# Kernel tuning notes

Measured on AMD Instinct MI355X. Metric: run time of the kernel, lower is better.

## Reference

```python
import jax, jax.numpy as jnp
import numpy as np

E = 2048      # embed_dim = qk_dim = v_dim = proj_dim
H = 16        # n_head
D = 128       # head_dim
ROT = 64      # rotary_dim (partial rotary: ROT < D)
PAD = 50257   # pad_token_id in select_at_last_token
EPS = 1e-5    # layer_norm_epsilon


def _sincos(T):
    # fixed_pos_embedding (GPT-J style): [T, ROT//2] each
    inv_freq = 1.0 / (10000.0 ** (jnp.arange(0, ROT, 2, dtype=jnp.float32) / ROT))
    ang = jnp.arange(T, dtype=jnp.float32)[:, None] * inv_freq[None, :]
    return jnp.sin(ang), jnp.cos(ang)


def _rope(x, sin, cos):
    # x: [B,T,H,ROT]; sin/cos: [T, ROT//2]; repeat_interleave(2) on last dim
    sin2 = jnp.repeat(sin, 2, axis=-1)[None, :, None, :]
    cos2 = jnp.repeat(cos, 2, axis=-1)[None, :, None, :]
    x1 = x[..., ::2]
    x2 = x[..., 1::2]
    rot = jnp.stack((-x2, x1), axis=-1).reshape(x.shape)  # rotate_every_two
    return x * cos2 + rot * sin2


def setup_inputs() -> dict:
    key = jax.random.key(0)
    ks = jax.random.split(key, 8)
    B, S = 8, 2048
    s = 0.02
    return {
        "hidden_states": jax.random.normal(ks[0], (B, S, E), jnp.float32),
        "input_ids_with_pads": jax.random.randint(ks[1], (B, S), 0, PAD),
        "ln_w": jnp.ones((E,), jnp.float32),
        "ln_b": jnp.zeros((E,), jnp.float32),
        "q_w": jax.random.normal(ks[2], (E, E), jnp.float32) * s,
        "q_b": jnp.zeros((E,), jnp.float32),
        "k_w": jax.random.normal(ks[3], (E, E), jnp.float32) * s,
        "k_b": jnp.zeros((E,), jnp.float32),
        "v_w": jax.random.normal(ks[4], (E, E), jnp.float32) * s,
        "v_b": jnp.zeros((E,), jnp.float32),
        "out_w": jax.random.normal(ks[5], (E, E), jnp.float32) * s,
        "out_b": jnp.zeros((E,), jnp.float32),
    }


def reference(hidden_states, input_ids_with_pads, ln_w, ln_b,
              q_w, q_b, k_w, k_b, v_w, v_b, out_w, out_b):
    B, S, _ = hidden_states.shape
    # LayerNorm
    mu = jnp.mean(hidden_states, axis=-1, keepdims=True)
    var = jnp.mean(jnp.square(hidden_states - mu), axis=-1, keepdims=True)
    hs = (hidden_states - mu) * jax.lax.rsqrt(var + EPS) * ln_w + ln_b
    # select_at_last_token: index of last non-pad token per row
    ix = jnp.argmax(jnp.cumsum((input_ids_with_pads != PAD).astype(jnp.int32), axis=1), axis=1)  # [B]
    h_last = jnp.take_along_axis(hs, ix[:, None, None], axis=1)  # [B,1,E]
    # projections (pool_to_vector: single query token)
    q = h_last @ q_w.T + q_b           # [B,1,E]
    k = hs @ k_w.T + k_b               # [B,S,E]
    v = hs @ v_w.T + v_b               # [B,S,E]
    # split heads; rotary layout keeps [B,T,H,D] for q,k
    q = q.reshape(B, 1, H, D)
    k = k.reshape(B, S, H, D)
    v = v.reshape(B, S, H, D).transpose(0, 2, 1, 3)  # [B,H,S,D]
    # partial rotary on first ROT dims (query at position 0, keys 0..S-1)
    sin, cos = _sincos(S)
    q = jnp.concatenate([_rope(q[..., :ROT], sin[:1], cos[:1]), q[..., ROT:]], axis=-1)
    k = jnp.concatenate([_rope(k[..., :ROT], sin, cos), k[..., ROT:]], axis=-1)
    q = q.transpose(0, 2, 1, 3)  # [B,H,1,D]
    k = k.transpose(0, 2, 1, 3)  # [B,H,S,D]
    # GPT-Neo _attn: no 1/sqrt(d) scaling; `bias` buffer is all-ones so the
    # causal mask is all-True and masked_bias is never applied.
    scores = jnp.einsum('bhqd,bhkd->bhqk', q, k)   # [B,H,1,S]
    attn = jax.nn.softmax(scores, axis=-1)
    out = jnp.einsum('bhqk,bhkd->bhqd', attn, v)   # [B,H,1,D]
    out = out.transpose(0, 2, 1, 3).reshape(B, 1, H * D)  # merge heads
    out = out @ out_w.T + out_b                    # out_proj
    return out[:, 0, :]                            # squeeze(-2): [B,E]
```

## Files before the change

kernel.cpp:

```cpp
#include <hip/hip_runtime.h>
#include <hip/hip_bf16.h>
#include <cstdint>
#include <cstddef>


using bf16x8 = __attribute__((ext_vector_type(8))) __bf16;
using f32x4  = __attribute__((ext_vector_type(4))) float;

__device__ __forceinline__ unsigned short f2bf(float f) {
  unsigned u = __float_as_uint(f);
  u += 0x7fffu + ((u >> 16) & 1u);
  return (unsigned short)(u >> 16);
}

__device__ __forceinline__ void gld16(const void* g, void* l) {
  __builtin_amdgcn_global_load_lds((__attribute__((address_space(1))) void*)g,
                                   (__attribute__((address_space(3))) void*)l,
                                   16, 0, 0);
}

#define FENCE() asm volatile("" ::: "memory")
#define SBAR()  { FENCE(); __builtin_amdgcn_s_barrier(); FENCE(); }
#define VM9()   asm volatile("s_waitcnt vmcnt(9)" ::: "memory")
#define VM8()   asm volatile("s_waitcnt vmcnt(8)" ::: "memory")
#define VM0()   asm volatile("s_waitcnt vmcnt(0)" ::: "memory")

__global__ __launch_bounds__(256) void prep_kernel(
    const float* __restrict__ hidden, const int* __restrict__ ids,
    const float* __restrict__ gw, const float* __restrict__ gb,
    const float* __restrict__ kw, unsigned short* __restrict__ hs,
    unsigned short* __restrict__ Wk, float2* __restrict__ tab,
    float* __restrict__ hl, float* __restrict__ Z) {
  const int blk = blockIdx.x, tid = threadIdx.x;
  const int wave = tid >> 6, lane = tid & 63;

  if (blk < 16384) {
    const size_t row = blk;
    const float* xr = hidden + row * 2048;
    float4 a = ((const float4*)xr)[tid];
    float4 b = ((const float4*)xr)[tid + 256];
    float s  = a.x + a.y + a.z + a.w + b.x + b.y + b.z + b.w;
    float ss = a.x*a.x + a.y*a.y + a.z*a.z + a.w*a.w +
               b.x*b.x + b.y*b.y + b.z*b.z + b.w*b.w;
    for (int m = 1; m < 64; m <<= 1) { s += __shfl_xor(s, m); ss += __shfl_xor(ss, m); }
    __shared__ float rs[4], rss[4];
    if (lane == 0) { rs[wave] = s; rss[wave] = ss; }
    __syncthreads();
    s  = rs[0] + rs[1] + rs[2] + rs[3];
    ss = rss[0] + rss[1] + rss[2] + rss[3];
    const float mu = s * (1.f / 2048.f);
    const float var = ss * (1.f / 2048.f) - mu * mu;
    const float r = rsqrtf(var + 1e-5f);
    const int i0 = tid * 4, i1 = 1024 + tid * 4;
    ushort4 p0 = {f2bf((a.x - mu) * r * gw[i0 + 0] + gb[i0 + 0]),
                  f2bf((a.y - mu) * r * gw[i0 + 1] + gb[i0 + 1]),
                  f2bf((a.z - mu) * r * gw[i0 + 2] + gb[i0 + 2]),
                  f2bf((a.w - mu) * r * gw[i0 + 3] + gb[i0 + 3])};
    ushort4 p1 = {f2bf((b.x - mu) * r * gw[i1 + 0] + gb[i1 + 0]),
                  f2bf((b.y - mu) * r * gw[i1 + 1] + gb[i1 + 1]),
                  f2bf((b.z - mu) * r * gw[i1 + 2] + gb[i1 + 2]),
                  f2bf((b.w - mu) * r * gw[i1 + 3] + gb[i1 + 3])};
    *(ushort4*)(hs + row * 2048 + i0) = p0;
    *(ushort4*)(hs + row * 2048 + i1) = p1;
  } else if (blk < 18432) {
    const size_t i4 = (size_t)(blk - 16384) * 256 + tid;
    const int r = (int)(i4 >> 9);
    const int col4 = (int)(i4 & 511);
    const size_t src4 = ((size_t)((r >> 6) * 128 + (r & 63))) * 512 + col4;
    float4 v = ((const float4*)kw)[src4];
    ushort4 o = {f2bf(v.x), f2bf(v.y), f2bf(v.z), f2bf(v.w)};
    ((ushort4*)Wk)[i4] = o;
  } else if (blk < 18688) {
    const int t = (blk - 18432) * 8 + (tid >> 5);
    const int i = tid & 31;
    const float inv = exp2f(-(float)i * (13.287712379549449f / 32.f));
    const float ang = (float)t * inv;
    tab[t * 32 + i] = make_float2(sinf(ang), cosf(ang));
  } else {
    const int b = blk - 18688;
    if (tid < 16) Z[b * 16 + tid] = 0.f;
    int best = -1;
    for (int t = tid; t < 2048; t += 256)
      if (ids[b * 2048 + t] != 50257) best = (t > best) ? t : best;
    for (int m = 1; m < 64; m <<= 1) {
      int o = __shfl_xor(best, m);
      best = (o > best) ? o : best;
    }
    __shared__ int rb[4];
    if (lane == 0) rb[wave] = best;
    __syncthreads();
    int ix = rb[0];
    for (int w = 1; w < 4; ++w) ix = (rb[w] > ix) ? rb[w] : ix;
    ix = (ix < 0) ? 0 : ix;
    const float* xr = hidden + ((size_t)b * 2048 + ix) * 2048;
    float4 a = ((const float4*)xr)[tid];
    float4 c = ((const float4*)xr)[tid + 256];
    float s  = a.x + a.y + a.z + a.w + c.x + c.y + c.z + c.w;
    float ss = a.x*a.x + a.y*a.y + a.z*a.z + a.w*a.w +
               c.x*c.x + c.y*c.y + c.z*c.z + c.w*c.w;
    for (int m = 1; m < 64; m <<= 1) { s += __shfl_xor(s, m); ss += __shfl_xor(ss, m); }
    __shared__ float rs2[4], rss2[4];
    if (lane == 0) { rs2[wave] = s; rss2[wave] = ss; }
    __syncthreads();
    s  = rs2[0] + rs2[1] + rs2[2] + rs2[3];
    ss = rss2[0] + rss2[1] + rss2[2] + rss2[3];
    const float mu = s * (1.f / 2048.f);
    const float var = ss * (1.f / 2048.f) - mu * mu;
    const float r = rsqrtf(var + 1e-5f);
    const int i0 = tid * 4, i1 = 1024 + tid * 4;
    float* yo = hl + (size_t)b * 2048;
    yo[i0 + 0] = (a.x - mu) * r * gw[i0 + 0] + gb[i0 + 0];
    yo[i0 + 1] = (a.y - mu) * r * gw[i0 + 1] + gb[i0 + 1];
    yo[i0 + 2] = (a.z - mu) * r * gw[i0 + 2] + gb[i0 + 2];
    yo[i0 + 3] = (a.w - mu) * r * gw[i0 + 3] + gb[i0 + 3];
    yo[i1 + 0] = (c.x - mu) * r * gw[i1 + 0] + gb[i1 + 0];
    yo[i1 + 1] = (c.y - mu) * r * gw[i1 + 1] + gb[i1 + 1];
    yo[i1 + 2] = (c.z - mu) * r * gw[i1 + 2] + gb[i1 + 2];
    yo[i1 + 3] = (c.w - mu) * r * gw[i1 + 3] + gb[i1 + 3];
  }
}

__global__ __launch_bounds__(256) void gemv8_kernel(const float* __restrict__ X,
                                                    const float* __restrict__ W,
                                                    const float* __restrict__ bias,
                                                    float* __restrict__ Y) {
  const int tid = threadIdx.x, lane = tid & 63, wave = tid >> 6;
  const int e = blockIdx.x * 4 + wave;
  const float* wr = W + (size_t)e * 2048;
  float p[8] = {0, 0, 0, 0, 0, 0, 0, 0};
#pragma unroll
  for (int it = 0; it < 8; ++it) {
    const int k = it * 256 + lane * 4;
    float4 wv = *(const float4*)(wr + k);
#pragma unroll
    for (int b = 0; b < 8; ++b) {
      float4 xv = *(const float4*)(X + b * 2048 + k);
      p[b] += wv.x * xv.x + wv.y * xv.y + wv.z * xv.z + wv.w * xv.w;
    }
  }
#pragma unroll
  for (int b = 0; b < 8; ++b)
    for (int m = 1; m < 64; m <<= 1) p[b] += __shfl_xor(p[b], m);
  if (lane == 0) {
    const float bb = bias[e];
#pragma unroll
    for (int b = 0; b < 8; ++b) Y[(size_t)b * 2048 + e] = p[b] + bb;
  }
}

__global__ __launch_bounds__(256) void fold_c_kernel(
    const float* __restrict__ qv, const float* __restrict__ kw,
    const float* __restrict__ kb, unsigned short* __restrict__ Cpad,
    float* __restrict__ qkb) {
  const int bh = blockIdx.x, b = bh >> 4, h = bh & 15;
  const int tid = threadIdx.x;
  const float* qh = qv + ((size_t)b * 16 + h) * 128 + 64;
  const int e0 = tid * 8;
  float acc[8] = {0, 0, 0, 0, 0, 0, 0, 0};
  for (int c = 0; c < 64; ++c) {
    const float qc = qh[c];
    const float* row = kw + ((size_t)(h * 128 + 64 + c)) * 2048 + e0;
    float4 v0 = *(const float4*)(row);
    float4 v1 = *(const float4*)(row + 4);
    acc[0] += qc * v0.x; acc[1] += qc * v0.y; acc[2] += qc * v0.z; acc[3] += qc * v0.w;
    acc[4] += qc * v1.x; acc[5] += qc * v1.y; acc[6] += qc * v1.z; acc[7] += qc * v1.w;
  }
  unsigned short* dst = Cpad + ((size_t)b * 128 + h) * 2048 + e0;
  ushort4 o0 = {f2bf(acc[0]), f2bf(acc[1]), f2bf(acc[2]), f2bf(acc[3])};
  ushort4 o1 = {f2bf(acc[4]), f2bf(acc[5]), f2bf(acc[6]), f2bf(acc[7])};
  *(ushort4*)(dst) = o0;
  *(ushort4*)(dst + 4) = o1;
  if (tid < 64) {
    float p = kb[h * 128 + 64 + tid] * qh[tid];
    for (int m = 1; m < 64; m <<= 1) p += __shfl_xor(p, m);
    if (tid == 0) qkb[bh] = p;
  }
}

__global__ __launch_bounds__(512, 2) void gemm_kscore_rot_kernel(
    const unsigned short* __restrict__ A, const unsigned short* __restrict__ W,
    const unsigned short* __restrict__ Cpad, const float* __restrict__ qkb,
    const float* __restrict__ kb, const float* __restrict__ qv,
    const float2* __restrict__ tab, float* __restrict__ sw_t,
    float* __restrict__ Z) {
  constexpr int K = 2048;
  constexpr int NT = K / 64;
  __shared__ unsigned short Ls[4 * 16384 + 2 * 1024];

  const int tid = threadIdx.x;
  const int lane = tid & 63, wave = tid >> 6;
  const int wr = wave >> 2, wc = wave & 3;
  const int l15 = lane & 15, lk = lane >> 4, l7 = lane & 7;

  const int orig = blockIdx.x;
  const int wgid = (orig & 7) * 32 + (orig >> 3);
  const int bm = wgid >> 2;
  const int bn = wgid & 3;
  const int b  = bm >> 3;

  const int srow = tid >> 3;
  const int scb  = (tid & 7) ^ (srow & 7);
  const unsigned short* Asrc = A + ((size_t)(bm * 256 + srow)) * K + scb * 8;
  const unsigned short* Bsrc = W + ((size_t)(bn * 256 + srow)) * K + scb * 8;
  const int crow = (lane >> 3) & 3;
  const int ccb  = (lane & 7) ^ (crow & 7);
  const unsigned short* Csrc =
      Cpad + ((size_t)(b * 128 + bn * 4 + crow)) * K + ccb * 8;
  const int wave512 = wave * 512;
  unsigned short* Lc = Ls + 65536;

  f32x4 acc[8][4];
  f32x4 accc[8];
#pragma unroll
  for (int i = 0; i < 8; ++i) {
    accc[i] = (f32x4){0.f, 0.f, 0.f, 0.f};
#pragma unroll
    for (int j = 0; j < 4; ++j) acc[i][j] = (f32x4){0.f, 0.f, 0.f, 0.f};
  }

  int rowA[8], rowB[4];
#pragma unroll
  for (int mi = 0; mi < 8; ++mi) rowA[mi] = (wr * 128 + mi * 16 + l15) * 64;
#pragma unroll
  for (int nj = 0; nj < 4; ++nj) rowB[nj] = (wc * 64 + nj * 16 + l15) * 64;
  const int rowC = l15 * 64;

#pragma unroll
  for (int p = 0; p < 4; ++p) {
    gld16(Asrc + (size_t)p * 64 * K, Ls + p * 4096 + wave512);
    gld16(Bsrc + (size_t)p * 64 * K, Ls + 16384 + p * 4096 + wave512);
  }
  if (wave == 0 && lane < 32) gld16(Csrc, Lc);
#pragma unroll
  for (int p = 0; p < 4; ++p) {
    gld16(Asrc + (size_t)p * 64 * K + 64, Ls + 32768 + p * 4096 + wave512);
    gld16(Bsrc + (size_t)p * 64 * K + 64, Ls + 49152 + p * 4096 + wave512);
  }
  if (wave == 0 && lane < 32) gld16(Csrc + 64, Lc + 1024);
  if (wave == 0) { VM9(); } else { VM8(); }
  SBAR();

  for (int t = 0; t < NT; ++t) {
    const unsigned short* bufA = Ls + (t & 1) * 32768;
    const unsigned short* bufB = bufA + 16384;
    const unsigned short* bufC = Lc + (t & 1) * 1024;
#pragma unroll
    for (int ks = 0; ks < 2; ++ks) {
      const int offk = ((((ks << 2) | lk) ^ l7) << 3);
      bf16x8 af[8], bfr[4], cf;
#pragma unroll
      for (int mi = 0; mi < 8; ++mi)
        af[mi] = *(const bf16x8*)(bufA + rowA[mi] + offk);
#pragma unroll
      for (int nj = 0; nj < 4; ++nj)
        bfr[nj] = *(const bf16x8*)(bufB + rowB[nj] + offk);
      cf = *(const bf16x8*)(bufC + rowC + offk);
      __builtin_amdgcn_s_setprio(1);
#pragma unroll
      for (int mi = 0; mi < 8; ++mi) {
        accc[mi] = __builtin_amdgcn_mfma_f32_16x16x32_bf16(af[mi], cf,
                                                           accc[mi], 0, 0, 0);
#pragma unroll
        for (int nj = 0; nj < 4; ++nj)
          acc[mi][nj] = __builtin_amdgcn_mfma_f32_16x16x32_bf16(
              af[mi], bfr[nj], acc[mi][nj], 0, 0, 0);
      }
      __builtin_amdgcn_s_setprio(0);
    }
    if (t == NT - 1) break;
    SBAR();
    if (t + 2 < NT) {
      const int k0 = (t + 2) * 64;
      unsigned short* dA = Ls + (t & 1) * 32768 + wave512;
      unsigned short* dB = dA + 16384;
#pragma unroll
      for (int p = 0; p < 4; ++p) {
        gld16(Asrc + (size_t)p * 64 * K + k0, dA + p * 4096);
        gld16(Bsrc + (size_t)p * 64 * K + k0, dB + p * 4096);
      }
      if (wave == 0 && lane < 32) gld16(Csrc + k0, Lc + (t & 1) * 1024);
      if (wave == 0) { VM9(); } else { VM8(); }
    } else {
      VM0();
    }
    SBAR();
  }

  const int h  = bn * 4 + wc;
  const int rg = lk;
  const float* qb  = qv + ((size_t)b * 16 + h) * 128;
  const float* kbh = kb + h * 128;
  const float qkbv = qkb[b * 16 + h];
  float rowsum[8][4];
#pragma unroll
  for (int mi = 0; mi < 8; ++mi)
#pragma unroll
    for (int r = 0; r < 4; ++r) rowsum[mi][r] = 0.f;

  const int s0g = bm * 256 + wr * 128;
  const float sgn = (l15 & 1) ? -1.f : 1.f;
#pragma unroll
  for (int nj = 0; nj < 4; ++nj) {
    const int c = nj * 16 + l15;
    const float qd   = qb[c];
    const float qps  = sgn * qb[c ^ 1];
    const float bias = kbh[c];
    const int i = c >> 1;
#pragma unroll
    for (int mi = 0; mi < 8; ++mi)
#pragma unroll
      for (int r = 0; r < 4; ++r) {
        const int t = s0g + mi * 16 + rg * 4 + r;
        const float2 sc = tab[(t & 2047) * 32 + i];
        rowsum[mi][r] += (acc[mi][nj][r] + bias) * (qd * sc.y + qps * sc.x);
      }
  }
#pragma unroll
  for (int mi = 0; mi < 8; ++mi)
#pragma unroll
    for (int r = 0; r < 4; ++r) {
      float v = rowsum[mi][r];
      v += __shfl_xor(v, 1);
      v += __shfl_xor(v, 2);
      v += __shfl_xor(v, 4);
      v += __shfl_xor(v, 8);
      rowsum[mi][r] = v;
    }
  const int srcl = (lane & 48) | wc;
#pragma unroll
  for (int mi = 0; mi < 8; ++mi)
#pragma unroll
    for (int r = 0; r < 4; ++r)
      rowsum[mi][r] += __shfl(accc[mi][r], srcl) + qkbv;

  float zpart = 0.f;
  if (l15 == 0) {
#pragma unroll
    for (int mi = 0; mi < 8; ++mi)
#pragma unroll
      for (int r = 0; r < 4; ++r) {
        const int gr = s0g + mi * 16 + rg * 4 + r;
        const float w = __expf(rowsum[mi][r] - 40.f);
        sw_t[(size_t)gr * 16 + h] = w;
        zpart += w;
      }
    zpart += __shfl_xor(zpart, 16);
    zpart += __shfl_xor(zpart, 32);
    if (lane == 0) atomicAdd(&Z[b * 16 + h], zpart);
  }
}

__global__ __launch_bounds__(256) void attn_wsum_kernel(
    const unsigned short* __restrict__ hs, const float* __restrict__ sw_t,
    float* __restrict__ part) {
  const int b = blockIdx.x, ech = blockIdx.y, tc = blockIdx.z;
  const int tid = threadIdx.x;
  const int e = ech * 512 + tid * 2;
  __shared__ float sw[128 * 16];
  {
    const float4* src = (const float4*)(sw_t + ((size_t)b * 2048 + tc * 128) * 16);
    float4* dst = (float4*)sw;
    dst[tid] = src[tid];
    dst[tid + 256] = src[tid + 256];
  }
  __syncthreads();
  float a0[16], a1[16];
#pragma unroll
  for (int h = 0; h < 16; ++h) { a0[h] = 0.f; a1[h] = 0.f; }
  const unsigned short* hp = hs + ((size_t)b * 2048 + tc * 128) * 2048 + e;
#pragma unroll 2
  for (int tt = 0; tt < 128; ++tt) {
    const unsigned hv = *(const unsigned*)(hp + (size_t)tt * 2048);
    const float h0 = __uint_as_float(hv << 16);
    const float h1 = __uint_as_float(hv & 0xffff0000u);
    const float4 w0 = *(const float4*)(sw + tt * 16 + 0);
    const float4 w1 = *(const float4*)(sw + tt * 16 + 4);
    const float4 w2 = *(const float4*)(sw + tt * 16 + 8);
    const float4 w3 = *(const float4*)(sw + tt * 16 + 12);
    const float wv[16] = {w0.x, w0.y, w0.z, w0.w, w1.x, w1.y, w1.z, w1.w,
                          w2.x, w2.y, w2.z, w2.w, w3.x, w3.y, w3.z, w3.w};
#pragma unroll
    for (int h = 0; h < 16; ++h) {
      a0[h] += wv[h] * h0;
      a1[h] += wv[h] * h1;
    }
  }
#pragma unroll
  for (int h = 0; h < 16; ++h) {
    float2 st = {a0[h], a1[h]};
    *(float2*)(part + (((size_t)tc * 8 + b) * 16 + h) * 2048 + e) = st;
  }
}

__global__ __launch_bounds__(256) void attn_comb_kernel(
    const float* __restrict__ part, const float* __restrict__ Z,
    float* __restrict__ wsumN) {
  const int bh = blockIdx.x, b = bh >> 4, h = bh & 15;
  const float zi = 1.f / Z[bh];
  for (int e = threadIdx.x; e < 2048; e += 256) {
    float s = 0.f;
#pragma unroll
    for (int tc = 0; tc < 16; ++tc)
      s += part[(((size_t)tc * 8 + b) * 16 + h) * 2048 + e];
    wsumN[(size_t)bh * 2048 + e] = s * zi;
  }
}

__global__ __launch_bounds__(256) void attn_vgemv_kernel(
    const float* __restrict__ vw, const float* __restrict__ vb,
    const float* __restrict__ wsumN, float* __restrict__ aout) {
  const int tid = threadIdx.x, lane = tid & 63, wave = tid >> 6;
  const int gw = blockIdx.x * 4 + wave;
  const int h = gw >> 7, d = gw & 127;
  const float* vr = vw + (size_t)gw * 2048;
  float p[8] = {0, 0, 0, 0, 0, 0, 0, 0};
#pragma unroll
  for (int it = 0; it < 8; ++it) {
    const int k = it * 256 + lane * 4;
    float4 wv = *(const float4*)(vr + k);
#pragma unroll
    for (int b = 0; b < 8; ++b) {
      float4 xv = *(const float4*)(wsumN + ((size_t)b * 16 + h) * 2048 + k);
      p[b] += wv.x * xv.x + wv.y * xv.y + wv.z * xv.z + wv.w * xv.w;
    }
  }
#pragma unroll
  for (int b = 0; b < 8; ++b)
    for (int m = 1; m < 64; m <<= 1) p[b] += __shfl_xor(p[b], m);
  if (lane == 0) {
    const float bb = vb[gw];
#pragma unroll
    for (int b = 0; b < 8; ++b)
      aout[((size_t)b * 16 + h) * 128 + d] = p[b] + bb;
  }
}

extern "C" void kernel_launch(void* const* d_in, const int* in_sizes, int n_in,
                              void* d_out, int out_size, void* d_ws, size_t ws_size,
                              hipStream_t stream) {
  (void)in_sizes; (void)n_in; (void)out_size; (void)ws_size;
  const float* hidden = (const float*)d_in[0];
  const int*   ids    = (const int*)d_in[1];
  const float* ln_w   = (const float*)d_in[2];
  const float* ln_b   = (const float*)d_in[3];
  const float* q_w    = (const float*)d_in[4];
  const float* q_b    = (const float*)d_in[5];
  const float* k_w    = (const float*)d_in[6];
  const float* k_b    = (const float*)d_in[7];
  const float* v_w    = (const float*)d_in[8];
  const float* v_b    = (const float*)d_in[9];
  const float* out_w  = (const float*)d_in[10];
  const float* out_b  = (const float*)d_in[11];
  float* out = (float*)d_out;

  char* ws = (char*)d_ws;
  unsigned short* hs  = (unsigned short*)ws; ws += (size_t)16384 * 2048 * 2;
  unsigned short* Wk  = (unsigned short*)ws; ws += (size_t)1024 * 2048 * 2;
  unsigned short* Cpad = (unsigned short*)ws; ws += (size_t)8 * 128 * 2048 * 2;
  float2* sctab = (float2*)ws; ws += (size_t)2048 * 32 * 8;
  float* qv     = (float*)ws; ws += (size_t)8 * 2048 * 4;
  float* hl     = (float*)ws; ws += (size_t)8 * 2048 * 4;
  float* aout   = (float*)ws; ws += (size_t)8 * 2048 * 4;
  float* sw_t   = (float*)ws; ws += (size_t)8 * 2048 * 16 * 4;
  float* qkb    = (float*)ws; ws += 128 * 4;
  float* Zb     = (float*)ws; ws += 128 * 4;
  float* part   = (float*)ws; ws += (size_t)16 * 8 * 16 * 2048 * 4;
  float* wsumN  = (float*)ws; ws += (size_t)128 * 2048 * 4;

  prep_kernel<<<18696, 256, 0, stream>>>(hidden, ids, ln_w, ln_b, k_w,
                                         hs, Wk, sctab, hl, Zb);
  gemv8_kernel<<<512, 256, 0, stream>>>(hl, q_w, q_b, qv);
  fold_c_kernel<<<128, 256, 0, stream>>>(qv, k_w, k_b, Cpad, qkb);
  gemm_kscore_rot_kernel<<<256, 512, 0, stream>>>(hs, Wk, Cpad, qkb, k_b, qv,
                                                  sctab, sw_t, Zb);
  attn_wsum_kernel<<<dim3(8, 4, 16), 256, 0, stream>>>(hs, sw_t, part);
  attn_comb_kernel<<<128, 256, 0, stream>>>(part, Zb, wsumN);
  attn_vgemv_kernel<<<512, 256, 0, stream>>>(v_b ? v_w : v_w, v_b, wsumN, aout);
  gemv8_kernel<<<512, 256, 0, stream>>>(aout, out_w, out_b, out);
}
```

Measured before the change: 401.2 us.

## Fuse q-projection with C fold and replace partial-sum combine with atomics

Merges the q GEMV and the fold_c kernel into a single per-(batch,head) qhead kernel that stages the last-token hidden row in LDS. The attention weighted-sum kernel now covers 256 tokens per block and atomically adds into a wsumN buffer that prep zeroes, so the partial buffer and the combine kernel are gone. The 1/Z normalisation moves into the V GEMV epilogue. This cuts the launch count and partial-buffer traffic, at the cost of float atomics (nondeterministic summation order) and a q GEMV that runs on only 128 threads per block with redundant weight reads across batches.

Result: slower. 474.5 us (+18.3%).

```diff
diff --git a/kernel.cpp b/kernel.cpp
--- a/kernel.cpp
+++ b/kernel.cpp
@@ -30,7 +30,8 @@
     const float* __restrict__ gw, const float* __restrict__ gb,
     const float* __restrict__ kw, unsigned short* __restrict__ hs,
     unsigned short* __restrict__ Wk, float2* __restrict__ tab,
-    float* __restrict__ hl, float* __restrict__ Z) {
+    float* __restrict__ hl, float* __restrict__ Z,
+    float* __restrict__ wsumN) {
   const int blk = blockIdx.x, tid = threadIdx.x;
   const int wave = tid >> 6, lane = tid & 63;
 
@@ -76,7 +77,7 @@
     const float inv = exp2f(-(float)i * (13.287712379549449f / 32.f));
     const float ang = (float)t * inv;
     tab[t * 32 + i] = make_float2(sinf(ang), cosf(ang));
-  } else {
+  } else if (blk < 18696) {
     const int b = blk - 18688;
     if (tid < 16) Z[b * 16 + tid] = 0.f;
     int best = -1;
@@ -117,6 +118,58 @@
     yo[i1 + 1] = (c.y - mu) * r * gw[i1 + 1] + gb[i1 + 1];
     yo[i1 + 2] = (c.z - mu) * r * gw[i1 + 2] + gb[i1 + 2];
     yo[i1 + 3] = (c.w - mu) * r * gw[i1 + 3] + gb[i1 + 3];
+  } else {
+    const int idx = (blk - 18696) * 256 + tid;
+    ((float4*)wsumN)[idx] = (float4){0.f, 0.f, 0.f, 0.f};
+  }
+}
+
+__global__ __launch_bounds__(256) void qhead_kernel(
+    const float* __restrict__ hl, const float* __restrict__ qw,
+    const float* __restrict__ qbias, const float* __restrict__ kw,
+    const float* __restrict__ kb, float* __restrict__ qv,
+    unsigned short* __restrict__ Cpad, float* __restrict__ qkb) {
+  const int bh = blockIdx.x, b = bh >> 4, h = bh & 15;
+  const int tid = threadIdx.x;
+  __shared__ float hls[2048];
+  __shared__ float qsh[64];
+  ((float4*)hls)[tid]       = ((const float4*)(hl + (size_t)b * 2048))[tid];
+  ((float4*)hls)[tid + 256] = ((const float4*)(hl + (size_t)b * 2048))[tid + 256];
+  __syncthreads();
+  if (tid < 128) {
+    const float* wr = qw + (size_t)(h * 128 + tid) * 2048;
+    float4 a = {0.f, 0.f, 0.f, 0.f};
+#pragma unroll 4
+    for (int k = 0; k < 512; ++k) {
+      const float4 wv = ((const float4*)wr)[k];
+      const float4 xv = *(const float4*)(hls + k * 4);
+      a.x += wv.x * xv.x; a.y += wv.y * xv.y;
+      a.z += wv.z * xv.z; a.w += wv.w * xv.w;
+    }
+    const float q = a.x + a.y + a.z + a.w + qbias[h * 128 + tid];
+    qv[(size_t)bh * 128 + tid] = q;
+    if (tid >= 64) qsh[tid - 64] = q;
+  }
+  __syncthreads();
+  const int e0 = tid * 8;
+  float acc[8] = {0, 0, 0, 0, 0, 0, 0, 0};
+  for (int c = 0; c < 64; ++c) {
+    const float qc = qsh[c];
+    const float* row = kw + ((size_t)(h * 128 + 64 + c)) * 2048 + e0;
+    float4 v0 = *(const float4*)(row);
+    float4 v1 = *(const float4*)(row + 4);
+    acc[0] += qc * v0.x; acc[1] += qc * v0.y; acc[2] += qc * v0.z; acc[3] += qc * v0.w;
+    acc[4] += qc * v1.x; acc[5] += qc * v1.y; acc[6] += qc * v1.z; acc[7] += qc * v1.w;
+  }
+  unsigned short* dst = Cpad + ((size_t)b * 128 + h) * 2048 + e0;
+  ushort4 o0 = {f2bf(acc[0]), f2bf(acc[1]), f2bf(acc[2]), f2bf(acc[3])};
+  ushort4 o1 = {f2bf(acc[4]), f2bf(acc[5]), f2bf(acc[6]), f2bf(acc[7])};
+  *(ushort4*)(dst) = o0;
+  *(ushort4*)(dst + 4) = o1;
+  if (tid < 64) {
+    float p = kb[h * 128 + 64 + tid] * qsh[tid];
+    for (int m = 1; m < 64; m <<= 1) p += __shfl_xor(p, m);
+    if (tid == 0) qkb[bh] = p;
   }
 }
 
@@ -145,35 +198,6 @@
     const float bb = bias[e];
 #pragma unroll
     for (int b = 0; b < 8; ++b) Y[(size_t)b * 2048 + e] = p[b] + bb;
-  }
-}
-
-__global__ __launch_bounds__(256) void fold_c_kernel(
-    const float* __restrict__ qv, const float* __restrict__ kw,
-    const float* __restrict__ kb, unsigned short* __restrict__ Cpad,
-    float* __restrict__ qkb) {
-  const int bh = blockIdx.x, b = bh >> 4, h = bh & 15;
-  const int tid = threadIdx.x;
-  const float* qh = qv + ((size_t)b * 16 + h) * 128 + 64;
-  const int e0 = tid * 8;
-  float acc[8] = {0, 0, 0, 0, 0, 0, 0, 0};
-  for (int c = 0; c < 64; ++c) {
-    const float qc = qh[c];
-    const float* row = kw + ((size_t)(h * 128 + 64 + c)) * 2048 + e0;
-    float4 v0 = *(const float4*)(row);
-    float4 v1 = *(const float4*)(row + 4);
-    acc[0] += qc * v0.x; acc[1] += qc * v0.y; acc[2] += qc * v0.z; acc[3] += qc * v0.w;
-    acc[4] += qc * v1.x; acc[5] += qc * v1.y; acc[6] += qc * v1.z; acc[7] += qc * v1.w;
-  }
-  unsigned short* dst = Cpad + ((size_t)b * 128 + h) * 2048 + e0;
-  ushort4 o0 = {f2bf(acc[0]), f2bf(acc[1]), f2bf(acc[2]), f2bf(acc[3])};
-  ushort4 o1 = {f2bf(acc[4]), f2bf(acc[5]), f2bf(acc[6]), f2bf(acc[7])};
-  *(ushort4*)(dst) = o0;
-  *(ushort4*)(dst + 4) = o1;
-  if (tid < 64) {
-    float p = kb[h * 128 + 64 + tid] * qh[tid];
-    for (int m = 1; m < 64; m <<= 1) p += __shfl_xor(p, m);
-    if (tid == 0) qkb[bh] = p;
   }
 }
 
@@ -352,24 +376,24 @@
 
 __global__ __launch_bounds__(256) void attn_wsum_kernel(
     const unsigned short* __restrict__ hs, const float* __restrict__ sw_t,
-    float* __restrict__ part) {
+    float* __restrict__ wsumN) {
   const int b = blockIdx.x, ech = blockIdx.y, tc = blockIdx.z;
   const int tid = threadIdx.x;
   const int e = ech * 512 + tid * 2;
-  __shared__ float sw[128 * 16];
+  __shared__ float sw[256 * 16];
   {
-    const float4* src = (const float4*)(sw_t + ((size_t)b * 2048 + tc * 128) * 16);
+    const float4* src = (const float4*)(sw_t + ((size_t)b * 2048 + tc * 256) * 16);
     float4* dst = (float4*)sw;
-    dst[tid] = src[tid];
-    dst[tid + 256] = src[tid + 256];
+#pragma unroll
+    for (int i = 0; i < 4; ++i) dst[tid + i * 256] = src[tid + i * 256];
   }
   __syncthreads();
   float a0[16], a1[16];
 #pragma unroll
   for (int h = 0; h < 16; ++h) { a0[h] = 0.f; a1[h] = 0.f; }
-  const unsigned short* hp = hs + ((size_t)b * 2048 + tc * 128) * 2048 + e;
+  const unsigned short* hp = hs + ((size_t)b * 2048 + tc * 256) * 2048 + e;
 #pragma unroll 2
-  for (int tt = 0; tt < 128; ++tt) {
+  for (int tt = 0; tt < 256; ++tt) {
     const unsigned hv = *(const unsigned*)(hp + (size_t)tt * 2048);
     const float h0 = __uint_as_float(hv << 16);
     const float h1 = __uint_as_float(hv & 0xffff0000u);
@@ -387,28 +411,16 @@
   }
 #pragma unroll
   for (int h = 0; h < 16; ++h) {
-    float2 st = {a0[h], a1[h]};
-    *(float2*)(part + (((size_t)tc * 8 + b) * 16 + h) * 2048 + e) = st;
-  }
-}
-
-__global__ __launch_bounds__(256) void attn_comb_kernel(
-    const float* __restrict__ part, const float* __restrict__ Z,
-    float* __restrict__ wsumN) {
-  const int bh = blockIdx.x, b = bh >> 4, h = bh & 15;
-  const float zi = 1.f / Z[bh];
-  for (int e = threadIdx.x; e < 2048; e += 256) {
-    float s = 0.f;
-#pragma unroll
-    for (int tc = 0; tc < 16; ++tc)
-      s += part[(((size_t)tc * 8 + b) * 16 + h) * 2048 + e];
-    wsumN[(size_t)bh * 2048 + e] = s * zi;
+    float* dst = wsumN + ((size_t)b * 16 + h) * 2048 + e;
+    atomicAdd(dst, a0[h]);
+    atomicAdd(dst + 1, a1[h]);
   }
 }
 
 __global__ __launch_bounds__(256) void attn_vgemv_kernel(
     const float* __restrict__ vw, const float* __restrict__ vb,
-    const float* __restrict__ wsumN, float* __restrict__ aout) {
+    const float* __restrict__ wsumN, const float* __restrict__ Z,
+    float* __restrict__ aout) {
   const int tid = threadIdx.x, lane = tid & 63, wave = tid >> 6;
   const int gw = blockIdx.x * 4 + wave;
   const int h = gw >> 7, d = gw & 127;
@@ -431,7 +443,7 @@
     const float bb = vb[gw];
 #pragma unroll
     for (int b = 0; b < 8; ++b)
-      aout[((size_t)b * 16 + h) * 128 + d] = p[b] + bb;
+      aout[((size_t)b * 16 + h) * 128 + d] = p[b] / Z[b * 16 + h] + bb;
   }
 }
 
@@ -464,17 +476,15 @@
   float* sw_t   = (float*)ws; ws += (size_t)8 * 2048 * 16 * 4;
   float* qkb    = (float*)ws; ws += 128 * 4;
   float* Zb     = (float*)ws; ws += 128 * 4;
-  float* part   = (float*)ws; ws += (size_t)16 * 8 * 16 * 2048 * 4;
   float* wsumN  = (float*)ws; ws += (size_t)128 * 2048 * 4;
 
-  prep_kernel<<<18696, 256, 0, stream>>>(hidden, ids, ln_w, ln_b, k_w,
-                                         hs, Wk, sctab, hl, Zb);
-  gemv8_kernel<<<512, 256, 0, stream>>>(hl, q_w, q_b, qv);
-  fold_c_kernel<<<128, 256, 0, stream>>>(qv, k_w, k_b, Cpad, qkb);
+  prep_kernel<<<18952, 256, 0, stream>>>(hidden, ids, ln_w, ln_b, k_w,
+                                         hs, Wk, sctab, hl, Zb, wsumN);
+  qhead_kernel<<<128, 256, 0, stream>>>(hl, q_w, q_b, k_w, k_b,
+                                        qv, Cpad, qkb);
   gemm_kscore_rot_kernel<<<256, 512, 0, stream>>>(hs, Wk, Cpad, qkb, k_b, qv,
                                                   sctab, sw_t, Zb);
-  attn_wsum_kernel<<<dim3(8, 4, 16), 256, 0, stream>>>(hs, sw_t, part);
-  attn_comb_kernel<<<128, 256, 0, stream>>>(part, Zb, wsumN);
-  attn_vgemv_kernel<<<512, 256, 0, stream>>>(v_b ? v_w : v_w, v_b, wsumN, aout);
+  attn_wsum_kernel<<<dim3(8, 4, 8), 256, 0, stream>>>(hs, sw_t, wsumN);
+  attn_vgemv_kernel<<<512, 256, 0, stream>>>(v_w, v_b, wsumN, Zb, aout);
   gemv8_kernel<<<512, 256, 0, stream>>>(aout, out_w, out_b, out);
 }
```

## Replace partial-sum buffer and combine kernel with atomic accumulation

Applied to the files above, without the earlier changes.

The weighted-sum kernel now accumulates its per-chunk results straight into wsumN with float atomicAdd instead of writing a 16-way partial buffer, and the separate combine kernel is removed. The 1/Z normalisation moves into the V GEMV epilogue, and wsumN is zeroed by extra blocks in the prep kernel. This drops one launch plus a 16 MB partial write and read, at the cost of 16-way atomic contention per element and a summation order that is no longer deterministic.

After: 419.2 us. +4.5%, slower.

```diff
diff --git a/kernel.cpp b/kernel.cpp
--- a/kernel.cpp
+++ b/kernel.cpp
@@ -30,7 +30,8 @@
     const float* __restrict__ gw, const float* __restrict__ gb,
     const float* __restrict__ kw, unsigned short* __restrict__ hs,
     unsigned short* __restrict__ Wk, float2* __restrict__ tab,
-    float* __restrict__ hl, float* __restrict__ Z) {
+    float* __restrict__ hl, float* __restrict__ Z,
+    float* __restrict__ wsumN) {
   const int blk = blockIdx.x, tid = threadIdx.x;
   const int wave = tid >> 6, lane = tid & 63;
 
@@ -76,7 +77,7 @@
     const float inv = exp2f(-(float)i * (13.287712379549449f / 32.f));
     const float ang = (float)t * inv;
     tab[t * 32 + i] = make_float2(sinf(ang), cosf(ang));
-  } else {
+  } else if (blk < 18696) {
     const int b = blk - 18688;
     if (tid < 16) Z[b * 16 + tid] = 0.f;
     int best = -1;
@@ -117,6 +118,9 @@
     yo[i1 + 1] = (c.y - mu) * r * gw[i1 + 1] + gb[i1 + 1];
     yo[i1 + 2] = (c.z - mu) * r * gw[i1 + 2] + gb[i1 + 2];
     yo[i1 + 3] = (c.w - mu) * r * gw[i1 + 3] + gb[i1 + 3];
+  } else {
+    const int idx = (blk - 18696) * 256 + tid;
+    ((float4*)wsumN)[idx] = (float4){0.f, 0.f, 0.f, 0.f};
   }
 }
 
@@ -352,7 +356,7 @@
 
 __global__ __launch_bounds__(256) void attn_wsum_kernel(
     const unsigned short* __restrict__ hs, const float* __restrict__ sw_t,
-    float* __restrict__ part) {
+    float* __restrict__ wsumN) {
   const int b = blockIdx.x, ech = blockIdx.y, tc = blockIdx.z;
   const int tid = threadIdx.x;
   const int e = ech * 512 + tid * 2;
@@ -387,28 +391,16 @@
   }
 #pragma unroll
   for (int h = 0; h < 16; ++h) {
-    float2 st = {a0[h], a1[h]};
-    *(float2*)(part + (((size_t)tc * 8 + b) * 16 + h) * 2048 + e) = st;
-  }
-}
-
-__global__ __launch_bounds__(256) void attn_comb_kernel(
-    const float* __restrict__ part, const float* __restrict__ Z,
-    float* __restrict__ wsumN) {
-  const int bh = blockIdx.x, b = bh >> 4, h = bh & 15;
-  const float zi = 1.f / Z[bh];
-  for (int e = threadIdx.x; e < 2048; e += 256) {
-    float s = 0.f;
-#pragma unroll
-    for (int tc = 0; tc < 16; ++tc)
-      s += part[(((size_t)tc * 8 + b) * 16 + h) * 2048 + e];
-    wsumN[(size_t)bh * 2048 + e] = s * zi;
+    float* dst = wsumN + ((size_t)b * 16 + h) * 2048 + e;
+    atomicAdd(dst, a0[h]);
+    atomicAdd(dst + 1, a1[h]);
   }
 }
 
 __global__ __launch_bounds__(256) void attn_vgemv_kernel(
     const float* __restrict__ vw, const float* __restrict__ vb,
-    const float* __restrict__ wsumN, float* __restrict__ aout) {
+    const float* __restrict__ wsumN, const float* __restrict__ Z,
+    float* __restrict__ aout) {
   const int tid = threadIdx.x, lane = tid & 63, wave = tid >> 6;
   const int gw = blockIdx.x * 4 + wave;
   const int h = gw >> 7, d = gw & 127;
@@ -431,7 +423,7 @@
     const float bb = vb[gw];
 #pragma unroll
     for (int b = 0; b < 8; ++b)
-      aout[((size_t)b * 16 + h) * 128 + d] = p[b] + bb;
+      aout[((size_t)b * 16 + h) * 128 + d] = p[b] / Z[b * 16 + h] + bb;
   }
 }
 
@@ -464,17 +456,15 @@
   float* sw_t   = (float*)ws; ws += (size_t)8 * 2048 * 16 * 4;
   float* qkb    = (float*)ws; ws += 128 * 4;
   float* Zb     = (float*)ws; ws += 128 * 4;
-  float* part   = (float*)ws; ws += (size_t)16 * 8 * 16 * 2048 * 4;
   float* wsumN  = (float*)ws; ws += (size_t)128 * 2048 * 4;
 
-  prep_kernel<<<18696, 256, 0, stream>>>(hidden, ids, ln_w, ln_b, k_w,
-                                         hs, Wk, sctab, hl, Zb);
+  prep_kernel<<<18952, 256, 0, stream>>>(hidden, ids, ln_w, ln_b, k_w,
+                                         hs, Wk, sctab, hl, Zb, wsumN);
   gemv8_kernel<<<512, 256, 0, stream>>>(hl, q_w, q_b, qv);
   fold_c_kernel<<<128, 256, 0, stream>>>(qv, k_w, k_b, Cpad, qkb);
   gemm_kscore_rot_kernel<<<256, 512, 0, stream>>>(hs, Wk, Cpad, qkb, k_b, qv,
                                                   sctab, sw_t, Zb);
-  attn_wsum_kernel<<<dim3(8, 4, 16), 256, 0, stream>>>(hs, sw_t, part);
-  attn_comb_kernel<<<128, 256, 0, stream>>>(part, Zb, wsumN);
-  attn_vgemv_kernel<<<512, 256, 0, stream>>>(v_b ? v_w : v_w, v_b, wsumN, aout);
+  attn_wsum_kernel<<<dim3(8, 4, 16), 256, 0, stream>>>(hs, sw_t, wsumN);
+  attn_vgemv_kernel<<<512, 256, 0, stream>>>(v_w, v_b, wsumN, Zb, aout);
   gemv8_kernel<<<512, 256, 0, stream>>>(aout, out_w, out_b, out);
 }
```

## Switch K-score GEMM to triple-buffered BK=32 pipeline; split fold_c across two blocks

Applied to the files above, without the earlier changes.

The main K-projection/score GEMM now uses K-tiles of 32 with three LDS buffers instead of two 64-wide buffers. The next stage's loads are issued at the top of each iteration, before the MFMAs, so one barrier per iteration is removed and load latency can overlap compute. The XOR swizzle on LDS rows is dropped, which may bring back bank conflicts on the 64-byte row reads. fold_c is split into two half-row blocks per (batch, head), doubling the grid so more CUs share the weight reads.

Result: no change. 406.3 us (+1.3%).

```diff
diff --git a/kernel.cpp b/kernel.cpp
--- a/kernel.cpp
+++ b/kernel.cpp
@@ -21,8 +21,8 @@
 
 #define FENCE() asm volatile("" ::: "memory")
 #define SBAR()  { FENCE(); __builtin_amdgcn_s_barrier(); FENCE(); }
-#define VM9()   asm volatile("s_waitcnt vmcnt(9)" ::: "memory")
-#define VM8()   asm volatile("s_waitcnt vmcnt(8)" ::: "memory")
+#define VM5()   asm volatile("s_waitcnt vmcnt(5)" ::: "memory")
+#define VM4()   asm volatile("s_waitcnt vmcnt(4)" ::: "memory")
 #define VM0()   asm volatile("s_waitcnt vmcnt(0)" ::: "memory")
 
 __global__ __launch_bounds__(256) void prep_kernel(
@@ -152,25 +152,21 @@
     const float* __restrict__ qv, const float* __restrict__ kw,
     const float* __restrict__ kb, unsigned short* __restrict__ Cpad,
     float* __restrict__ qkb) {
-  const int bh = blockIdx.x, b = bh >> 4, h = bh & 15;
+  const int blk = blockIdx.x, bh = blk >> 1, half = blk & 1;
+  const int b = bh >> 4, h = bh & 15;
   const int tid = threadIdx.x;
   const float* qh = qv + ((size_t)b * 16 + h) * 128 + 64;
-  const int e0 = tid * 8;
-  float acc[8] = {0, 0, 0, 0, 0, 0, 0, 0};
+  const int e0 = half * 1024 + tid * 4;
+  float acc[4] = {0, 0, 0, 0};
+#pragma unroll 4
   for (int c = 0; c < 64; ++c) {
     const float qc = qh[c];
-    const float* row = kw + ((size_t)(h * 128 + 64 + c)) * 2048 + e0;
-    float4 v0 = *(const float4*)(row);
-    float4 v1 = *(const float4*)(row + 4);
-    acc[0] += qc * v0.x; acc[1] += qc * v0.y; acc[2] += qc * v0.z; acc[3] += qc * v0.w;
-    acc[4] += qc * v1.x; acc[5] += qc * v1.y; acc[6] += qc * v1.z; acc[7] += qc * v1.w;
-  }
-  unsigned short* dst = Cpad + ((size_t)b * 128 + h) * 2048 + e0;
-  ushort4 o0 = {f2bf(acc[0]), f2bf(acc[1]), f2bf(acc[2]), f2bf(acc[3])};
-  ushort4 o1 = {f2bf(acc[4]), f2bf(acc[5]), f2bf(acc[6]), f2bf(acc[7])};
-  *(ushort4*)(dst) = o0;
-  *(ushort4*)(dst + 4) = o1;
-  if (tid < 64) {
+    const float4 v = *(const float4*)(kw + ((size_t)(h * 128 + 64 + c)) * 2048 + e0);
+    acc[0] += qc * v.x; acc[1] += qc * v.y; acc[2] += qc * v.z; acc[3] += qc * v.w;
+  }
+  ushort4 o = {f2bf(acc[0]), f2bf(acc[1]), f2bf(acc[2]), f2bf(acc[3])};
+  *(ushort4*)(Cpad + ((size_t)b * 128 + h) * 2048 + e0) = o;
+  if (half == 0 && tid < 64) {
     float p = kb[h * 128 + 64 + tid] * qh[tid];
     for (int m = 1; m < 64; m <<= 1) p += __shfl_xor(p, m);
     if (tid == 0) qkb[bh] = p;
@@ -184,13 +180,13 @@
     const float2* __restrict__ tab, float* __restrict__ sw_t,
     float* __restrict__ Z) {
   constexpr int K = 2048;
-  constexpr int NT = K / 64;
-  __shared__ unsigned short Ls[4 * 16384 + 2 * 1024];
+  constexpr int NT = K / 32;
+  __shared__ unsigned short Ls[3 * 16384 + 3 * 512];
 
   const int tid = threadIdx.x;
   const int lane = tid & 63, wave = tid >> 6;
   const int wr = wave >> 2, wc = wave & 3;
-  const int l15 = lane & 15, lk = lane >> 4, l7 = lane & 7;
+  const int l15 = lane & 15, lk = lane >> 4;
 
   const int orig = blockIdx.x;
   const int wgid = (orig & 7) * 32 + (orig >> 3);
@@ -198,16 +194,12 @@
   const int bn = wgid & 3;
   const int b  = bm >> 3;
 
-  const int srow = tid >> 3;
-  const int scb  = (tid & 7) ^ (srow & 7);
-  const unsigned short* Asrc = A + ((size_t)(bm * 256 + srow)) * K + scb * 8;
-  const unsigned short* Bsrc = W + ((size_t)(bn * 256 + srow)) * K + scb * 8;
-  const int crow = (lane >> 3) & 3;
-  const int ccb  = (lane & 7) ^ (crow & 7);
+  const unsigned short* Asrc = A + ((size_t)(bm * 256 + (tid >> 2))) * K + (tid & 3) * 8;
+  const unsigned short* Bsrc = W + ((size_t)(bn * 256 + (tid >> 2))) * K + (tid & 3) * 8;
   const unsigned short* Csrc =
-      Cpad + ((size_t)(b * 128 + bn * 4 + crow)) * K + ccb * 8;
+      Cpad + ((size_t)(b * 128 + bn * 4 + ((lane >> 2) & 3))) * K + (lane & 3) * 8;
   const int wave512 = wave * 512;
-  unsigned short* Lc = Ls + 65536;
+  unsigned short* Lc = Ls + 49152;
 
   f32x4 acc[8][4];
   f32x4 accc[8];
@@ -220,71 +212,61 @@
 
   int rowA[8], rowB[4];
 #pragma unroll
-  for (int mi = 0; mi < 8; ++mi) rowA[mi] = (wr * 128 + mi * 16 + l15) * 64;
-#pragma unroll
-  for (int nj = 0; nj < 4; ++nj) rowB[nj] = (wc * 64 + nj * 16 + l15) * 64;
-  const int rowC = l15 * 64;
-
-#pragma unroll
-  for (int p = 0; p < 4; ++p) {
-    gld16(Asrc + (size_t)p * 64 * K, Ls + p * 4096 + wave512);
-    gld16(Bsrc + (size_t)p * 64 * K, Ls + 16384 + p * 4096 + wave512);
-  }
-  if (wave == 0 && lane < 32) gld16(Csrc, Lc);
-#pragma unroll
-  for (int p = 0; p < 4; ++p) {
-    gld16(Asrc + (size_t)p * 64 * K + 64, Ls + 32768 + p * 4096 + wave512);
-    gld16(Bsrc + (size_t)p * 64 * K + 64, Ls + 49152 + p * 4096 + wave512);
-  }
-  if (wave == 0 && lane < 32) gld16(Csrc + 64, Lc + 1024);
-  if (wave == 0) { VM9(); } else { VM8(); }
+  for (int mi = 0; mi < 8; ++mi) rowA[mi] = (wr * 128 + mi * 16 + l15) * 32;
+#pragma unroll
+  for (int nj = 0; nj < 4; ++nj) rowB[nj] = (wc * 64 + nj * 16 + l15) * 32;
+  const int rowC = l15 * 32;
+  const int lko  = lk * 8;
+
+#define STAGE(bufi, kb_) {                                                  \
+    unsigned short* d_ = Ls + (bufi) * 16384 + wave512;                     \
+    gld16(Asrc + (kb_),            d_);                                     \
+    gld16(Asrc + 128 * K + (kb_),  d_ + 4096);                              \
+    gld16(Bsrc + (kb_),            d_ + 8192);                              \
+    gld16(Bsrc + 128 * K + (kb_),  d_ + 12288);                             \
+    if (wave == 0) gld16(Csrc + (kb_), Lc + (bufi) * 512); }
+
+  STAGE(0, 0);
+  STAGE(1, 32);
+  if (wave == 0) { VM5(); } else { VM4(); }
   SBAR();
 
+  int cur = 0, ib = 2;
   for (int t = 0; t < NT; ++t) {
-    const unsigned short* bufA = Ls + (t & 1) * 32768;
-    const unsigned short* bufB = bufA + 16384;
-    const unsigned short* bufC = Lc + (t & 1) * 1024;
-#pragma unroll
-    for (int ks = 0; ks < 2; ++ks) {
-      const int offk = ((((ks << 2) | lk) ^ l7) << 3);
-      bf16x8 af[8], bfr[4], cf;
-#pragma unroll
-      for (int mi = 0; mi < 8; ++mi)
-        af[mi] = *(const bf16x8*)(bufA + rowA[mi] + offk);
+    if (t + 2 < NT) STAGE(ib, (t + 2) * 32);
+    const unsigned short* bufA = Ls + cur * 16384;
+    const unsigned short* bufB = bufA + 8192;
+    const unsigned short* bufC = Lc + cur * 512;
+    bf16x8 af[8], bfr[4], cf;
+#pragma unroll
+    for (int mi = 0; mi < 8; ++mi)
+      af[mi] = *(const bf16x8*)(bufA + rowA[mi] + lko);
+#pragma unroll
+    for (int nj = 0; nj < 4; ++nj)
+      bfr[nj] = *(const bf16x8*)(bufB + rowB[nj] + lko);
+    cf = *(const bf16x8*)(bufC + rowC + lko);
+    __builtin_amdgcn_s_setprio(1);
+#pragma unroll
+    for (int mi = 0; mi < 8; ++mi) {
+      accc[mi] = __builtin_amdgcn_mfma_f32_16x16x32_bf16(af[mi], cf,
+                                                         accc[mi], 0, 0, 0);
 #pragma unroll
       for (int nj = 0; nj < 4; ++nj)
-        bfr[nj] = *(const bf16x8*)(bufB + rowB[nj] + offk);
-      cf = *(const bf16x8*)(bufC + rowC + offk);
-      __builtin_amdgcn_s_setprio(1);
-#pragma unroll
-      for (int mi = 0; mi < 8; ++mi) {
-        accc[mi] = __builtin_amdgcn_mfma_f32_16x16x32_bf16(af[mi], cf,
-                                                           accc[mi], 0, 0, 0);
-#pragma unroll
-        for (int nj = 0; nj < 4; ++nj)
-          acc[mi][nj] = __builtin_amdgcn_mfma_f32_16x16x32_bf16(
-              af[mi], bfr[nj], acc[mi][nj], 0, 0, 0);
-      }
-      __builtin_amdgcn_s_setprio(0);
-    }
+        acc[mi][nj] = __builtin_amdgcn_mfma_f32_16x16x32_bf16(
+            af[mi], bfr[nj], acc[mi][nj], 0, 0, 0);
+    }
+    __builtin_amdgcn_s_setprio(0);
     if (t == NT - 1) break;
-    SBAR();
     if (t + 2 < NT) {
-      const int k0 = (t + 2) * 64;
-      unsigned short* dA = Ls + (t & 1) * 32768 + wave512;
-      unsigned short* dB = dA + 16384;
-#pragma unroll
-      for (int p = 0; p < 4; ++p) {
-        gld16(Asrc + (size_t)p * 64 * K + k0, dA + p * 4096);
-        gld16(Bsrc + (size_t)p * 64 * K + k0, dB + p * 4096);
-      }
-      if (wave == 0 && lane < 32) gld16(Csrc + k0, Lc + (t & 1) * 1024);
-      if (wave == 0) { VM9(); } else { VM8(); }
+      if (wave == 0) { VM5(); } else { VM4(); }
     } else {
       VM0();
     }
     SBAR();
-  }
+    cur = (cur == 2) ? 0 : cur + 1;
+    ib  = (ib == 2) ? 0 : ib + 1;
+  }
+#undef STAGE
 
   const int h  = bn * 4 + wc;
   const int rg = lk;
@@ -470,11 +452,11 @@
   prep_kernel<<<18696, 256, 0, stream>>>(hidden, ids, ln_w, ln_b, k_w,
                                          hs, Wk, sctab, hl, Zb);
   gemv8_kernel<<<512, 256, 0, stream>>>(hl, q_w, q_b, qv);
-  fold_c_kernel<<<128, 256, 0, stream>>>(qv, k_w, k_b, Cpad, qkb);
+  fold_c_kernel<<<256, 256, 0, stream>>>(qv, k_w, k_b, Cpad, qkb);
   gemm_kscore_rot_kernel<<<256, 512, 0, stream>>>(hs, Wk, Cpad, qkb, k_b, qv,
                                                   sctab, sw_t, Zb);
   attn_wsum_kernel<<<dim3(8, 4, 16), 256, 0, stream>>>(hs, sw_t, part);
   attn_comb_kernel<<<128, 256, 0, stream>>>(part, Zb, wsumN);
-  attn_vgemv_kernel<<<512, 256, 0, stream>>>(v_b ? v_w : v_w, v_b, wsumN, aout);
+  attn_vgemv_kernel<<<512, 256, 0, stream>>>(v_w, v_b, wsumN, aout);
   gemv8_kernel<<<512, 256, 0, stream>>>(aout, out_w, out_b, out);
 }
```
